# Optimization experiments

Hardware: AMD Instinct MI355X
Metric: run time of the kernel (lower is better)

The kernel has to match this reference:

```python
import jax, jax.numpy as jnp
import numpy as np

B, H, S, D = 2, 16, 2048, 64

def setup_inputs() -> dict:
    key = jax.random.key(0)
    kq, kk, kv = jax.random.split(key, 3)
    q = jax.random.normal(kq, (B, H, S, D), dtype=jnp.float32)
    k = jax.random.normal(kk, (B, H, S, D), dtype=jnp.float32)
    v = jax.random.normal(kv, (B, H, S, D), dtype=jnp.float32)
    # causal mask: True where position j > i (future tokens are masked)
    mask = jnp.triu(jnp.ones((S, S), dtype=bool), k=1)[None, None, :, :]
    return {"q": q, "k": k, "v": v, "mask": mask}

def reference(q, k, v, mask) -> jnp.ndarray:
    # scaled dot-product attention with additive -1e4 mask bias
    scale = 1.0 / jnp.sqrt(jnp.asarray(q.shape[-1], q.dtype))
    scores = jnp.einsum('bhqd,bhkd->bhqk', q, k) * scale  # [B,H,S,S]
    scores = scores + mask.astype(scores.dtype) * jnp.asarray(-10000.0, scores.dtype)
    probs = jax.nn.softmax(scores, axis=-1)
    # dropout is identity in eval mode
    return jnp.einsum('bhqk,bhkd->bhqd', probs, v)
```

## Files before the change

kernel.cpp:

```cpp
#include <hip/hip_runtime.h>

typedef __bf16 bf16_t;
typedef bf16_t bf16x8 __attribute__((ext_vector_type(8)));
typedef bf16_t bf16x4 __attribute__((ext_vector_type(4)));
typedef float  floatx4 __attribute__((ext_vector_type(4)));

constexpr int Sq = 2048, Dq = 64;
constexpr int BQ = 128, BK = 64;
constexpr int NQT = Sq / BQ;
constexpr int STR = 72;
constexpr float SCALE_LOG2E = 0.125f * 1.44269504088896340736f;

__global__ __launch_bounds__(256, 2) void flash_attn_kernel(
    const float* __restrict__ Q, const float* __restrict__ K,
    const float* __restrict__ V, float* __restrict__ O)
{
    __shared__ bf16_t QPs[BQ][STR];
    __shared__ bf16_t Ks[BK][STR];
    __shared__ bf16_t VTs[Dq][STR];

    const int tid  = threadIdx.x;
    const int wave = tid >> 6;
    const int lane = tid & 63;
    const int quad = lane >> 4;
    const int l16  = lane & 15;

    const int b  = blockIdx.x;
    const int x  = b & 255;
    const int bh = (x & 7) | (((x >> 7) & 1) << 3) | (((b >> 8) & 1) << 4);
    const int qidx = (x >> 3) & 15;
    const int qt = (b >> 8) ? (NQT - 1 - qidx) : qidx;
    const int ktmax = 2 * qt + 1;
    const long base = (long)bh * Sq * Dq;

    const int r0 = tid >> 4;
    const int c4 = (tid & 15) * 4;
    const int h  = lane >> 3;
    const int jw = wave * 16;

    #pragma unroll
    for (int p = 0; p < 8; ++p) {
        const int row = p * 16 + r0;
        const float4 qv = *(const float4*)&Q[base + (long)(qt * BQ + row) * Dq + c4];
        bf16x4 w;
        w[0] = (bf16_t)(qv.x * SCALE_LOG2E); w[1] = (bf16_t)(qv.y * SCALE_LOG2E);
        w[2] = (bf16_t)(qv.z * SCALE_LOG2E); w[3] = (bf16_t)(qv.w * SCALE_LOG2E);
        *(bf16x4*)&QPs[row][c4] = w;
    }
    __syncthreads();

    bf16x8 aq[2][2];
    #pragma unroll
    for (int u = 0; u < 2; ++u) {
        #pragma unroll
        for (int hh = 0; hh < 2; ++hh)
            aq[u][hh] = *(const bf16x8*)&QPs[32 * wave + u * 16 + l16][hh * 32 + quad * 8];
    }

    float l_lane[2] = {0.f, 0.f};
    floatx4 o_acc[2][4];
    #pragma unroll
    for (int u = 0; u < 2; ++u)
        #pragma unroll
        for (int dt = 0; dt < 4; ++dt) o_acc[u][dt] = floatx4{0.f, 0.f, 0.f, 0.f};

    float4 kf[4];
    float  vf[4][4];
    #pragma unroll
    for (int p = 0; p < 4; ++p) {
        kf[p] = *(const float4*)&K[base + (long)(p * 16 + r0) * Dq + c4];
        const int j0 = jw + 4 * ((p + h) & 3);
        #pragma unroll
        for (int r = 0; r < 4; ++r)
            vf[p][r] = V[base + (long)(j0 + r) * Dq + lane];
    }

    for (int kt = 0; kt <= ktmax; ++kt) {
        __syncthreads();

        #pragma unroll
        for (int p = 0; p < 4; ++p) {
            bf16x4 w;
            w[0] = (bf16_t)kf[p].x; w[1] = (bf16_t)kf[p].y;
            w[2] = (bf16_t)kf[p].z; w[3] = (bf16_t)kf[p].w;
            *(bf16x4*)&Ks[p * 16 + r0][c4] = w;
            bf16x4 vw;
            vw[0] = (bf16_t)vf[p][0]; vw[1] = (bf16_t)vf[p][1];
            vw[2] = (bf16_t)vf[p][2]; vw[3] = (bf16_t)vf[p][3];
            *(bf16x4*)&VTs[lane][jw + 4 * ((p + h) & 3)] = vw;
        }
        __syncthreads();

        {
            const int kn = (kt < ktmax) ? (kt + 1) : ktmax;
            const long kb = base + (long)kn * BK * Dq;
            #pragma unroll
            for (int p = 0; p < 4; ++p) {
                kf[p] = *(const float4*)&K[kb + (long)(p * 16 + r0) * Dq + c4];
                const int j0 = jw + 4 * ((p + h) & 3);
                #pragma unroll
                for (int r = 0; r < 4; ++r)
                    vf[p][r] = V[kb + (long)(j0 + r) * Dq + lane];
            }
        }

        floatx4 acc[4][2];
        #pragma unroll
        for (int t = 0; t < 4; ++t) {
            const int krow = t * 16 + l16;
            bf16x8 ak0 = *(const bf16x8*)&Ks[krow][quad * 8];
            bf16x8 ak1 = *(const bf16x8*)&Ks[krow][32 + quad * 8];
            #pragma unroll
            for (int u = 0; u < 2; ++u) {
                acc[t][u] = floatx4{0.f, 0.f, 0.f, 0.f};
                acc[t][u] = __builtin_amdgcn_mfma_f32_16x16x32_bf16(ak0, aq[u][0], acc[t][u], 0, 0, 0);
                acc[t][u] = __builtin_amdgcn_mfma_f32_16x16x32_bf16(ak1, aq[u][1], acc[t][u], 0, 0, 0);
            }
        }

        if (kt >= 2 * qt) {
            #pragma unroll
            for (int u = 0; u < 2; ++u) {
                const int qr = qt * BQ + 32 * wave + u * 16 + l16;
                #pragma unroll
                for (int t = 0; t < 4; ++t) {
                    #pragma unroll
                    for (int i = 0; i < 4; ++i) {
                        if (kt * BK + t * 16 + quad * 4 + i > qr) acc[t][u][i] = -1e30f;
                    }
                }
            }
        }

        #pragma unroll
        for (int u = 0; u < 2; ++u) {
            float l_add = 0.f;
            #pragma unroll
            for (int t = 0; t < 4; ++t) {
                #pragma unroll
                for (int i = 0; i < 4; ++i) {
                    acc[t][u][i] = __builtin_amdgcn_exp2f(acc[t][u][i]);
                    l_add += acc[t][u][i];
                }
            }
            l_lane[u] += l_add;
        }

        #pragma unroll
        for (int u = 0; u < 2; ++u) {
            #pragma unroll
            for (int t = 0; t < 4; ++t) {
                bf16x4 pk;
                pk[0] = (bf16_t)acc[t][u][0]; pk[1] = (bf16_t)acc[t][u][1];
                pk[2] = (bf16_t)acc[t][u][2]; pk[3] = (bf16_t)acc[t][u][3];
                *(bf16x4*)&QPs[32 * wave + u * 16 + l16][t * 16 + quad * 4] = pk;
            }
        }

        bf16x8 ap[2][2];
        #pragma unroll
        for (int u = 0; u < 2; ++u) {
            #pragma unroll
            for (int hh = 0; hh < 2; ++hh)
                ap[u][hh] = *(const bf16x8*)&QPs[32 * wave + u * 16 + l16][hh * 32 + quad * 8];
        }
        #pragma unroll
        for (int dt = 0; dt < 4; ++dt) {
            const int dcol = dt * 16 + l16;
            bf16x8 bv0 = *(const bf16x8*)&VTs[dcol][quad * 8];
            bf16x8 bv1 = *(const bf16x8*)&VTs[dcol][32 + quad * 8];
            #pragma unroll
            for (int u = 0; u < 2; ++u) {
                o_acc[u][dt] = __builtin_amdgcn_mfma_f32_16x16x32_bf16(ap[u][0], bv0, o_acc[u][dt], 0, 0, 0);
                o_acc[u][dt] = __builtin_amdgcn_mfma_f32_16x16x32_bf16(ap[u][1], bv1, o_acc[u][dt], 0, 0, 0);
            }
        }
    }

    #pragma unroll
    for (int u = 0; u < 2; ++u) {
        float lsum = l_lane[u];
        lsum += __shfl_xor(lsum, 16);
        lsum += __shfl_xor(lsum, 32);
        #pragma unroll
        for (int i = 0; i < 4; ++i) {
            const float inv_l = 1.f / __shfl(lsum, quad * 4 + i, 16);
            const long row = (long)qt * BQ + 32 * wave + u * 16 + quad * 4 + i;
            #pragma unroll
            for (int dt = 0; dt < 4; ++dt) {
                O[base + row * Dq + dt * 16 + l16] = o_acc[u][dt][i] * inv_l;
            }
        }
    }
}

extern "C" void kernel_launch(void* const* d_in, const int* in_sizes, int n_in,
                              void* d_out, int out_size, void* d_ws, size_t ws_size,
                              hipStream_t stream)
{
    const float* q = (const float*)d_in[0];
    const float* k = (const float*)d_in[1];
    const float* v = (const float*)d_in[2];
    float* out = (float*)d_out;
    flash_attn_kernel<<<dim3(512, 1, 1), dim3(256, 1, 1), 0, stream>>>(q, k, v, out);
}
```

Baseline: 135.1 us.

## Split causal KV range across two blocks with pairwise q-tile balancing and combine pass

```diff
diff --git a/kernel.cpp b/kernel.cpp
--- a/kernel.cpp
+++ b/kernel.cpp
@@ -11,9 +11,10 @@
 constexpr int STR = 72;
 constexpr float SCALE_LOG2E = 0.125f * 1.44269504088896340736f;
 
-__global__ __launch_bounds__(256, 2) void flash_attn_kernel(
+__global__ __launch_bounds__(256, 2) void flash_attn_splitk(
     const float* __restrict__ Q, const float* __restrict__ K,
-    const float* __restrict__ V, float* __restrict__ O)
+    const float* __restrict__ V, float* __restrict__ O,
+    float* __restrict__ wsO, float* __restrict__ wsLA, float* __restrict__ wsLB)
 {
     __shared__ bf16_t QPs[BQ][STR];
     __shared__ bf16_t Ks[BK][STR];
@@ -25,75 +26,57 @@
     const int quad = lane >> 4;
     const int l16  = lane & 15;
 
-    const int b  = blockIdx.x;
-    const int x  = b & 255;
-    const int bh = (x & 7) | (((x >> 7) & 1) << 3) | (((b >> 8) & 1) << 4);
-    const int qidx = (x >> 3) & 15;
-    const int qt = (b >> 8) ? (NQT - 1 - qidx) : qidx;
-    const int ktmax = 2 * qt + 1;
+    const int b    = blockIdx.x;
+    const int half = b >> 8;
+    const int x    = b & 255;
+    const int bh   = (x & 7) | ((x >> 6) << 3);
+    const int pair = (x >> 3) & 7;
     const long base = (long)bh * Sq * Dq;
+
+    float* __restrict__ dstO = half ? wsO  : O;
+    float* __restrict__ wsL  = half ? wsLB : wsLA;
 
     const int r0 = tid >> 4;
     const int c4 = (tid & 15) * 4;
     const int h  = lane >> 3;
     const int jw = wave * 16;
 
-    #pragma unroll
-    for (int p = 0; p < 8; ++p) {
-        const int row = p * 16 + r0;
-        const float4 qv = *(const float4*)&Q[base + (long)(qt * BQ + row) * Dq + c4];
-        bf16x4 w;
-        w[0] = (bf16_t)(qv.x * SCALE_LOG2E); w[1] = (bf16_t)(qv.y * SCALE_LOG2E);
-        w[2] = (bf16_t)(qv.z * SCALE_LOG2E); w[3] = (bf16_t)(qv.w * SCALE_LOG2E);
-        *(bf16x4*)&QPs[row][c4] = w;
-    }
-    __syncthreads();
-
-    bf16x8 aq[2][2];
-    #pragma unroll
-    for (int u = 0; u < 2; ++u) {
-        #pragma unroll
-        for (int hh = 0; hh < 2; ++hh)
-            aq[u][hh] = *(const bf16x8*)&QPs[32 * wave + u * 16 + l16][hh * 32 + quad * 8];
-    }
-
-    float l_lane[2] = {0.f, 0.f};
-    floatx4 o_acc[2][4];
-    #pragma unroll
-    for (int u = 0; u < 2; ++u)
-        #pragma unroll
-        for (int dt = 0; dt < 4; ++dt) o_acc[u][dt] = floatx4{0.f, 0.f, 0.f, 0.f};
-
-    float4 kf[4];
-    float  vf[4][4];
-    #pragma unroll
-    for (int p = 0; p < 4; ++p) {
-        kf[p] = *(const float4*)&K[base + (long)(p * 16 + r0) * Dq + c4];
-        const int j0 = jw + 4 * ((p + h) & 3);
-        #pragma unroll
-        for (int r = 0; r < 4; ++r)
-            vf[p][r] = V[base + (long)(j0 + r) * Dq + lane];
-    }
-
-    for (int kt = 0; kt <= ktmax; ++kt) {
+    for (int tt = 0; tt < 2; ++tt) {
+        const int qt   = tt ? (NQT - 1 - pair) : pair;
+        const int nkt  = qt + 1;
+        const int ktbeg = half * nkt;
+
         __syncthreads();
 
         #pragma unroll
-        for (int p = 0; p < 4; ++p) {
+        for (int p = 0; p < 8; ++p) {
+            const int row = p * 16 + r0;
+            const float4 qv = *(const float4*)&Q[base + (long)(qt * BQ + row) * Dq + c4];
             bf16x4 w;
-            w[0] = (bf16_t)kf[p].x; w[1] = (bf16_t)kf[p].y;
-            w[2] = (bf16_t)kf[p].z; w[3] = (bf16_t)kf[p].w;
-            *(bf16x4*)&Ks[p * 16 + r0][c4] = w;
-            bf16x4 vw;
-            vw[0] = (bf16_t)vf[p][0]; vw[1] = (bf16_t)vf[p][1];
-            vw[2] = (bf16_t)vf[p][2]; vw[3] = (bf16_t)vf[p][3];
-            *(bf16x4*)&VTs[lane][jw + 4 * ((p + h) & 3)] = vw;
+            w[0] = (bf16_t)(qv.x * SCALE_LOG2E); w[1] = (bf16_t)(qv.y * SCALE_LOG2E);
+            w[2] = (bf16_t)(qv.z * SCALE_LOG2E); w[3] = (bf16_t)(qv.w * SCALE_LOG2E);
+            *(bf16x4*)&QPs[row][c4] = w;
         }
         __syncthreads();
 
+        bf16x8 aq[2][2];
+        #pragma unroll
+        for (int u = 0; u < 2; ++u)
+            #pragma unroll
+            for (int hh = 0; hh < 2; ++hh)
+                aq[u][hh] = *(const bf16x8*)&QPs[32 * wave + u * 16 + l16][hh * 32 + quad * 8];
+
+        float l_lane[2] = {0.f, 0.f};
+        floatx4 o_acc[2][4];
+        #pragma unroll
+        for (int u = 0; u < 2; ++u)
+            #pragma unroll
+            for (int dt = 0; dt < 4; ++dt) o_acc[u][dt] = floatx4{0.f, 0.f, 0.f, 0.f};
+
+        float4 kf[4];
+        float  vf[4][4];
         {
-            const int kn = (kt < ktmax) ? (kt + 1) : ktmax;
-            const long kb = base + (long)kn * BK * Dq;
+            const long kb = base + (long)ktbeg * BK * Dq;
             #pragma unroll
             for (int p = 0; p < 4; ++p) {
                 kf[p] = *(const float4*)&K[kb + (long)(p * 16 + r0) * Dq + c4];
@@ -104,94 +87,141 @@
             }
         }
 
-        floatx4 acc[4][2];
-        #pragma unroll
-        for (int t = 0; t < 4; ++t) {
-            const int krow = t * 16 + l16;
-            bf16x8 ak0 = *(const bf16x8*)&Ks[krow][quad * 8];
-            bf16x8 ak1 = *(const bf16x8*)&Ks[krow][32 + quad * 8];
+        for (int j = 0; j < nkt; ++j) {
+            const int kt = ktbeg + j;
+            __syncthreads();
+
+            #pragma unroll
+            for (int p = 0; p < 4; ++p) {
+                bf16x4 w;
+                w[0] = (bf16_t)kf[p].x; w[1] = (bf16_t)kf[p].y;
+                w[2] = (bf16_t)kf[p].z; w[3] = (bf16_t)kf[p].w;
+                *(bf16x4*)&Ks[p * 16 + r0][c4] = w;
+                bf16x4 vw;
+                vw[0] = (bf16_t)vf[p][0]; vw[1] = (bf16_t)vf[p][1];
+                vw[2] = (bf16_t)vf[p][2]; vw[3] = (bf16_t)vf[p][3];
+                *(bf16x4*)&VTs[lane][jw + 4 * ((p + h) & 3)] = vw;
+            }
+            __syncthreads();
+
+            {
+                const int kn = (j + 1 < nkt) ? (kt + 1) : kt;
+                const long kb = base + (long)kn * BK * Dq;
+                #pragma unroll
+                for (int p = 0; p < 4; ++p) {
+                    kf[p] = *(const float4*)&K[kb + (long)(p * 16 + r0) * Dq + c4];
+                    const int j0 = jw + 4 * ((p + h) & 3);
+                    #pragma unroll
+                    for (int r = 0; r < 4; ++r)
+                        vf[p][r] = V[kb + (long)(j0 + r) * Dq + lane];
+                }
+            }
+
+            floatx4 acc[4][2];
+            #pragma unroll
+            for (int t = 0; t < 4; ++t) {
+                const int krow = t * 16 + l16;
+                bf16x8 ak0 = *(const bf16x8*)&Ks[krow][quad * 8];
+                bf16x8 ak1 = *(const bf16x8*)&Ks[krow][32 + quad * 8];
+                #pragma unroll
+                for (int u = 0; u < 2; ++u) {
+                    acc[t][u] = floatx4{0.f, 0.f, 0.f, 0.f};
+                    acc[t][u] = __builtin_amdgcn_mfma_f32_16x16x32_bf16(ak0, aq[u][0], acc[t][u], 0, 0, 0);
+                    acc[t][u] = __builtin_amdgcn_mfma_f32_16x16x32_bf16(ak1, aq[u][1], acc[t][u], 0, 0, 0);
+                }
+            }
+
+            if (kt >= 2 * qt) {
+                #pragma unroll
+                for (int u = 0; u < 2; ++u) {
+                    const int qr = qt * BQ + 32 * wave + u * 16 + l16;
+                    #pragma unroll
+                    for (int t = 0; t < 4; ++t) {
+                        #pragma unroll
+                        for (int i = 0; i < 4; ++i) {
+                            if (kt * BK + t * 16 + quad * 4 + i > qr) acc[t][u][i] = -1e30f;
+                        }
+                    }
+                }
+            }
+
             #pragma unroll
             for (int u = 0; u < 2; ++u) {
-                acc[t][u] = floatx4{0.f, 0.f, 0.f, 0.f};
-                acc[t][u] = __builtin_amdgcn_mfma_f32_16x16x32_bf16(ak0, aq[u][0], acc[t][u], 0, 0, 0);
-                acc[t][u] = __builtin_amdgcn_mfma_f32_16x16x32_bf16(ak1, aq[u][1], acc[t][u], 0, 0, 0);
-            }
-        }
-
-        if (kt >= 2 * qt) {
-            #pragma unroll
-            for (int u = 0; u < 2; ++u) {
-                const int qr = qt * BQ + 32 * wave + u * 16 + l16;
+                float l_add = 0.f;
                 #pragma unroll
                 for (int t = 0; t < 4; ++t) {
                     #pragma unroll
                     for (int i = 0; i < 4; ++i) {
-                        if (kt * BK + t * 16 + quad * 4 + i > qr) acc[t][u][i] = -1e30f;
+                        acc[t][u][i] = __builtin_amdgcn_exp2f(acc[t][u][i]);
+                        l_add += acc[t][u][i];
                     }
                 }
+                l_lane[u] += l_add;
+            }
+
+            #pragma unroll
+            for (int u = 0; u < 2; ++u) {
+                #pragma unroll
+                for (int t = 0; t < 4; ++t) {
+                    bf16x4 pk;
+                    pk[0] = (bf16_t)acc[t][u][0]; pk[1] = (bf16_t)acc[t][u][1];
+                    pk[2] = (bf16_t)acc[t][u][2]; pk[3] = (bf16_t)acc[t][u][3];
+                    *(bf16x4*)&QPs[32 * wave + u * 16 + l16][t * 16 + quad * 4] = pk;
+                }
+            }
+
+            bf16x8 ap[2][2];
+            #pragma unroll
+            for (int u = 0; u < 2; ++u)
+                #pragma unroll
+                for (int hh = 0; hh < 2; ++hh)
+                    ap[u][hh] = *(const bf16x8*)&QPs[32 * wave + u * 16 + l16][hh * 32 + quad * 8];
+            #pragma unroll
+            for (int dt = 0; dt < 4; ++dt) {
+                const int dcol = dt * 16 + l16;
+                bf16x8 bv0 = *(const bf16x8*)&VTs[dcol][quad * 8];
+                bf16x8 bv1 = *(const bf16x8*)&VTs[dcol][32 + quad * 8];
+                #pragma unroll
+                for (int u = 0; u < 2; ++u) {
+                    o_acc[u][dt] = __builtin_amdgcn_mfma_f32_16x16x32_bf16(ap[u][0], bv0, o_acc[u][dt], 0, 0, 0);
+                    o_acc[u][dt] = __builtin_amdgcn_mfma_f32_16x16x32_bf16(ap[u][1], bv1, o_acc[u][dt], 0, 0, 0);
+                }
             }
         }
 
         #pragma unroll
         for (int u = 0; u < 2; ++u) {
-            float l_add = 0.f;
-            #pragma unroll
-            for (int t = 0; t < 4; ++t) {
-                #pragma unroll
-                for (int i = 0; i < 4; ++i) {
-                    acc[t][u][i] = __builtin_amdgcn_exp2f(acc[t][u][i]);
-                    l_add += acc[t][u][i];
-                }
-            }
-            l_lane[u] += l_add;
-        }
-
-        #pragma unroll
-        for (int u = 0; u < 2; ++u) {
-            #pragma unroll
-            for (int t = 0; t < 4; ++t) {
-                bf16x4 pk;
-                pk[0] = (bf16_t)acc[t][u][0]; pk[1] = (bf16_t)acc[t][u][1];
-                pk[2] = (bf16_t)acc[t][u][2]; pk[3] = (bf16_t)acc[t][u][3];
-                *(bf16x4*)&QPs[32 * wave + u * 16 + l16][t * 16 + quad * 4] = pk;
-            }
-        }
-
-        bf16x8 ap[2][2];
-        #pragma unroll
-        for (int u = 0; u < 2; ++u) {
-            #pragma unroll
-            for (int hh = 0; hh < 2; ++hh)
-                ap[u][hh] = *(const bf16x8*)&QPs[32 * wave + u * 16 + l16][hh * 32 + quad * 8];
-        }
-        #pragma unroll
-        for (int dt = 0; dt < 4; ++dt) {
-            const int dcol = dt * 16 + l16;
-            bf16x8 bv0 = *(const bf16x8*)&VTs[dcol][quad * 8];
-            bf16x8 bv1 = *(const bf16x8*)&VTs[dcol][32 + quad * 8];
-            #pragma unroll
-            for (int u = 0; u < 2; ++u) {
-                o_acc[u][dt] = __builtin_amdgcn_mfma_f32_16x16x32_bf16(ap[u][0], bv0, o_acc[u][dt], 0, 0, 0);
-                o_acc[u][dt] = __builtin_amdgcn_mfma_f32_16x16x32_bf16(ap[u][1], bv1, o_acc[u][dt], 0, 0, 0);
+            float lsum = l_lane[u];
+            lsum += __shfl_xor(lsum, 16);
+            lsum += __shfl_xor(lsum, 32);
+            if (quad == 0) {
+                wsL[(bh * NQT + qt) * BQ + 32 * wave + u * 16 + l16] = lsum;
+            }
+            #pragma unroll
+            for (int i = 0; i < 4; ++i) {
+                const long row = (long)qt * BQ + 32 * wave + u * 16 + quad * 4 + i;
+                #pragma unroll
+                for (int dt = 0; dt < 4; ++dt) {
+                    dstO[base + row * Dq + dt * 16 + l16] = o_acc[u][dt][i];
+                }
             }
         }
     }
-
-    #pragma unroll
-    for (int u = 0; u < 2; ++u) {
-        float lsum = l_lane[u];
-        lsum += __shfl_xor(lsum, 16);
-        lsum += __shfl_xor(lsum, 32);
-        #pragma unroll
-        for (int i = 0; i < 4; ++i) {
-            const float inv_l = 1.f / __shfl(lsum, quad * 4 + i, 16);
-            const long row = (long)qt * BQ + 32 * wave + u * 16 + quad * 4 + i;
-            #pragma unroll
-            for (int dt = 0; dt < 4; ++dt) {
-                O[base + row * Dq + dt * 16 + l16] = o_acc[u][dt][i] * inv_l;
-            }
-        }
-    }
+}
+
+__global__ __launch_bounds__(256) void combine_kernel(
+    float* __restrict__ O, const float* __restrict__ wsO,
+    const float* __restrict__ lA, const float* __restrict__ lB)
+{
+    const int g = blockIdx.x * 256 + threadIdx.x;
+    const int row = g >> 4;
+    const float inv = 1.f / (lA[row] + lB[row]);
+    const float4 a = ((const float4*)O)[g];
+    const float4 c = ((const float4*)wsO)[g];
+    float4 r;
+    r.x = (a.x + c.x) * inv; r.y = (a.y + c.y) * inv;
+    r.z = (a.z + c.z) * inv; r.w = (a.w + c.w) * inv;
+    ((float4*)O)[g] = r;
 }
 
 extern "C" void kernel_launch(void* const* d_in, const int* in_sizes, int n_in,
@@ -202,5 +232,9 @@
     const float* k = (const float*)d_in[1];
     const float* v = (const float*)d_in[2];
     float* out = (float*)d_out;
-    flash_attn_kernel<<<dim3(512, 1, 1), dim3(256, 1, 1), 0, stream>>>(q, k, v, out);
+    float* wsO = (float*)d_ws;
+    float* lA  = wsO + 4194304;
+    float* lB  = lA + 65536;
+    flash_attn_splitk<<<dim3(512, 1, 1), dim3(256, 1, 1), 0, stream>>>(q, k, v, out, wsO, lA, lB);
+    combine_kernel<<<dim3(4096, 1, 1), dim3(256, 1, 1), 0, stream>>>(out, wsO, lA, lB);
 }
```

New measurement: 140.1 us. 3.7% more time.

## Split causal attention KV range across blocks with atomic accumulation and normalize pass

Applied to the files above, without the earlier changes.

```diff
diff --git a/kernel.cpp b/kernel.cpp
--- a/kernel.cpp
+++ b/kernel.cpp
@@ -11,9 +11,10 @@
 constexpr int STR = 72;
 constexpr float SCALE_LOG2E = 0.125f * 1.44269504088896340736f;
 
-__global__ __launch_bounds__(256, 2) void flash_attn_kernel(
+__global__ __launch_bounds__(256, 4) void flash_attn_splitk(
     const float* __restrict__ Q, const float* __restrict__ K,
-    const float* __restrict__ V, float* __restrict__ O)
+    const float* __restrict__ V, float* __restrict__ O,
+    float* __restrict__ wsL)
 {
     __shared__ bf16_t QPs[BQ][STR];
     __shared__ bf16_t Ks[BK][STR];
@@ -26,172 +27,198 @@
     const int l16  = lane & 15;
 
     const int b  = blockIdx.x;
+    const int j  = b >> 8;
     const int x  = b & 255;
-    const int bh = (x & 7) | (((x >> 7) & 1) << 3) | (((b >> 8) & 1) << 4);
-    const int qidx = (x >> 3) & 15;
-    const int qt = (b >> 8) ? (NQT - 1 - qidx) : qidx;
-    const int ktmax = 2 * qt + 1;
+    const int bh = (x & 7) | ((x >> 6) << 3);
+    const int p  = (x >> 3) & 7;
     const long base = (long)bh * Sq * Dq;
+
+    const int c0 = 9 * j - (j / 3);
+    const int c1 = c0 + 9 - (j >> 1);
+    const int sA = 2 * p + 2;
 
     const int r0 = tid >> 4;
     const int c4 = (tid & 15) * 4;
     const int h  = lane >> 3;
     const int jw = wave * 16;
 
-    #pragma unroll
-    for (int p = 0; p < 8; ++p) {
-        const int row = p * 16 + r0;
-        const float4 qv = *(const float4*)&Q[base + (long)(qt * BQ + row) * Dq + c4];
-        bf16x4 w;
-        w[0] = (bf16_t)(qv.x * SCALE_LOG2E); w[1] = (bf16_t)(qv.y * SCALE_LOG2E);
-        w[2] = (bf16_t)(qv.z * SCALE_LOG2E); w[3] = (bf16_t)(qv.w * SCALE_LOG2E);
-        *(bf16x4*)&QPs[row][c4] = w;
-    }
-    __syncthreads();
-
-    bf16x8 aq[2][2];
-    #pragma unroll
-    for (int u = 0; u < 2; ++u) {
-        #pragma unroll
-        for (int hh = 0; hh < 2; ++hh)
-            aq[u][hh] = *(const bf16x8*)&QPs[32 * wave + u * 16 + l16][hh * 32 + quad * 8];
-    }
-
-    float l_lane[2] = {0.f, 0.f};
-    floatx4 o_acc[2][4];
-    #pragma unroll
-    for (int u = 0; u < 2; ++u)
-        #pragma unroll
-        for (int dt = 0; dt < 4; ++dt) o_acc[u][dt] = floatx4{0.f, 0.f, 0.f, 0.f};
-
-    float4 kf[4];
-    float  vf[4][4];
-    #pragma unroll
-    for (int p = 0; p < 4; ++p) {
-        kf[p] = *(const float4*)&K[base + (long)(p * 16 + r0) * Dq + c4];
-        const int j0 = jw + 4 * ((p + h) & 3);
-        #pragma unroll
-        for (int r = 0; r < 4; ++r)
-            vf[p][r] = V[base + (long)(j0 + r) * Dq + lane];
-    }
-
-    for (int kt = 0; kt <= ktmax; ++kt) {
+    for (int seg = 0; seg < 2; ++seg) {
+        int qt, k0, k1;
+        if (seg == 0) { qt = p;           k0 = c0;                    k1 = (c1 < sA) ? c1 : sA; }
+        else          { qt = NQT - 1 - p; k0 = (c0 > sA ? c0 : sA) - sA; k1 = c1 - sA; }
+        if (k0 >= k1) continue;
+
         __syncthreads();
 
         #pragma unroll
-        for (int p = 0; p < 4; ++p) {
+        for (int pp = 0; pp < 8; ++pp) {
+            const int row = pp * 16 + r0;
+            const float4 qv = *(const float4*)&Q[base + (long)(qt * BQ + row) * Dq + c4];
             bf16x4 w;
-            w[0] = (bf16_t)kf[p].x; w[1] = (bf16_t)kf[p].y;
-            w[2] = (bf16_t)kf[p].z; w[3] = (bf16_t)kf[p].w;
-            *(bf16x4*)&Ks[p * 16 + r0][c4] = w;
-            bf16x4 vw;
-            vw[0] = (bf16_t)vf[p][0]; vw[1] = (bf16_t)vf[p][1];
-            vw[2] = (bf16_t)vf[p][2]; vw[3] = (bf16_t)vf[p][3];
-            *(bf16x4*)&VTs[lane][jw + 4 * ((p + h) & 3)] = vw;
+            w[0] = (bf16_t)(qv.x * SCALE_LOG2E); w[1] = (bf16_t)(qv.y * SCALE_LOG2E);
+            w[2] = (bf16_t)(qv.z * SCALE_LOG2E); w[3] = (bf16_t)(qv.w * SCALE_LOG2E);
+            *(bf16x4*)&QPs[row][c4] = w;
         }
         __syncthreads();
 
+        bf16x8 aq[2][2];
+        #pragma unroll
+        for (int u = 0; u < 2; ++u)
+            #pragma unroll
+            for (int hh = 0; hh < 2; ++hh)
+                aq[u][hh] = *(const bf16x8*)&QPs[32 * wave + u * 16 + l16][hh * 32 + quad * 8];
+
+        float l_lane[2] = {0.f, 0.f};
+        floatx4 o_acc[2][4];
+        #pragma unroll
+        for (int u = 0; u < 2; ++u)
+            #pragma unroll
+            for (int dt = 0; dt < 4; ++dt) o_acc[u][dt] = floatx4{0.f, 0.f, 0.f, 0.f};
+
+        float4 kf[4];
+        float  vf[4][4];
         {
-            const int kn = (kt < ktmax) ? (kt + 1) : ktmax;
-            const long kb = base + (long)kn * BK * Dq;
-            #pragma unroll
-            for (int p = 0; p < 4; ++p) {
-                kf[p] = *(const float4*)&K[kb + (long)(p * 16 + r0) * Dq + c4];
-                const int j0 = jw + 4 * ((p + h) & 3);
+            const long kb = base + (long)k0 * BK * Dq;
+            #pragma unroll
+            for (int pp = 0; pp < 4; ++pp) {
+                kf[pp] = *(const float4*)&K[kb + (long)(pp * 16 + r0) * Dq + c4];
+                const int j0 = jw + 4 * ((pp + h) & 3);
                 #pragma unroll
                 for (int r = 0; r < 4; ++r)
-                    vf[p][r] = V[kb + (long)(j0 + r) * Dq + lane];
-            }
-        }
-
-        floatx4 acc[4][2];
-        #pragma unroll
-        for (int t = 0; t < 4; ++t) {
-            const int krow = t * 16 + l16;
-            bf16x8 ak0 = *(const bf16x8*)&Ks[krow][quad * 8];
-            bf16x8 ak1 = *(const bf16x8*)&Ks[krow][32 + quad * 8];
+                    vf[pp][r] = V[kb + (long)(j0 + r) * Dq + lane];
+            }
+        }
+
+        for (int kt = k0; kt < k1; ++kt) {
+            __syncthreads();
+
+            #pragma unroll
+            for (int pp = 0; pp < 4; ++pp) {
+                bf16x4 w;
+                w[0] = (bf16_t)kf[pp].x; w[1] = (bf16_t)kf[pp].y;
+                w[2] = (bf16_t)kf[pp].z; w[3] = (bf16_t)kf[pp].w;
+                *(bf16x4*)&Ks[pp * 16 + r0][c4] = w;
+                bf16x4 vw;
+                vw[0] = (bf16_t)vf[pp][0]; vw[1] = (bf16_t)vf[pp][1];
+                vw[2] = (bf16_t)vf[pp][2]; vw[3] = (bf16_t)vf[pp][3];
+                *(bf16x4*)&VTs[lane][jw + 4 * ((pp + h) & 3)] = vw;
+            }
+            __syncthreads();
+
+            {
+                const int kn = (kt + 1 < k1) ? (kt + 1) : kt;
+                const long kb = base + (long)kn * BK * Dq;
+                #pragma unroll
+                for (int pp = 0; pp < 4; ++pp) {
+                    kf[pp] = *(const float4*)&K[kb + (long)(pp * 16 + r0) * Dq + c4];
+                    const int j0 = jw + 4 * ((pp + h) & 3);
+                    #pragma unroll
+                    for (int r = 0; r < 4; ++r)
+                        vf[pp][r] = V[kb + (long)(j0 + r) * Dq + lane];
+                }
+            }
+
+            floatx4 acc[4][2];
+            #pragma unroll
+            for (int t = 0; t < 4; ++t) {
+                const int krow = t * 16 + l16;
+                bf16x8 ak0 = *(const bf16x8*)&Ks[krow][quad * 8];
+                bf16x8 ak1 = *(const bf16x8*)&Ks[krow][32 + quad * 8];
+                #pragma unroll
+                for (int u = 0; u < 2; ++u) {
+                    acc[t][u] = floatx4{0.f, 0.f, 0.f, 0.f};
+                    acc[t][u] = __builtin_amdgcn_mfma_f32_16x16x32_bf16(ak0, aq[u][0], acc[t][u], 0, 0, 0);
+                    acc[t][u] = __builtin_amdgcn_mfma_f32_16x16x32_bf16(ak1, aq[u][1], acc[t][u], 0, 0, 0);
+                }
+            }
+
+            if (kt >= 2 * qt) {
+                #pragma unroll
+                for (int u = 0; u < 2; ++u) {
+                    const int qr = qt * BQ + 32 * wave + u * 16 + l16;
+                    #pragma unroll
+                    for (int t = 0; t < 4; ++t) {
+                        #pragma unroll
+                        for (int i = 0; i < 4; ++i) {
+                            if (kt * BK + t * 16 + quad * 4 + i > qr) acc[t][u][i] = -1e30f;
+                        }
+                    }
+                }
+            }
+
             #pragma unroll
             for (int u = 0; u < 2; ++u) {
-                acc[t][u] = floatx4{0.f, 0.f, 0.f, 0.f};
-                acc[t][u] = __builtin_amdgcn_mfma_f32_16x16x32_bf16(ak0, aq[u][0], acc[t][u], 0, 0, 0);
-                acc[t][u] = __builtin_amdgcn_mfma_f32_16x16x32_bf16(ak1, aq[u][1], acc[t][u], 0, 0, 0);
-            }
-        }
-
-        if (kt >= 2 * qt) {
-            #pragma unroll
-            for (int u = 0; u < 2; ++u) {
-                const int qr = qt * BQ + 32 * wave + u * 16 + l16;
+                float l_add = 0.f;
                 #pragma unroll
                 for (int t = 0; t < 4; ++t) {
                     #pragma unroll
                     for (int i = 0; i < 4; ++i) {
-                        if (kt * BK + t * 16 + quad * 4 + i > qr) acc[t][u][i] = -1e30f;
+                        acc[t][u][i] = __builtin_amdgcn_exp2f(acc[t][u][i]);
+                        l_add += acc[t][u][i];
                     }
                 }
+                l_lane[u] += l_add;
+            }
+
+            #pragma unroll
+            for (int u = 0; u < 2; ++u) {
+                #pragma unroll
+                for (int t = 0; t < 4; ++t) {
+                    bf16x4 pk;
+                    pk[0] = (bf16_t)acc[t][u][0]; pk[1] = (bf16_t)acc[t][u][1];
+                    pk[2] = (bf16_t)acc[t][u][2]; pk[3] = (bf16_t)acc[t][u][3];
+                    *(bf16x4*)&QPs[32 * wave + u * 16 + l16][t * 16 + quad * 4] = pk;
+                }
+            }
+
+            bf16x8 ap[2][2];
+            #pragma unroll
+            for (int u = 0; u < 2; ++u)
+                #pragma unroll
+                for (int hh = 0; hh < 2; ++hh)
+                    ap[u][hh] = *(const bf16x8*)&QPs[32 * wave + u * 16 + l16][hh * 32 + quad * 8];
+            #pragma unroll
+            for (int dt = 0; dt < 4; ++dt) {
+                const int dcol = dt * 16 + l16;
+                bf16x8 bv0 = *(const bf16x8*)&VTs[dcol][quad * 8];
+                bf16x8 bv1 = *(const bf16x8*)&VTs[dcol][32 + quad * 8];
+                #pragma unroll
+                for (int u = 0; u < 2; ++u) {
+                    o_acc[u][dt] = __builtin_amdgcn_mfma_f32_16x16x32_bf16(ap[u][0], bv0, o_acc[u][dt], 0, 0, 0);
+                    o_acc[u][dt] = __builtin_amdgcn_mfma_f32_16x16x32_bf16(ap[u][1], bv1, o_acc[u][dt], 0, 0, 0);
+                }
             }
         }
 
         #pragma unroll
         for (int u = 0; u < 2; ++u) {
-            float l_add = 0.f;
-            #pragma unroll
-            for (int t = 0; t < 4; ++t) {
-                #pragma unroll
-                for (int i = 0; i < 4; ++i) {
-                    acc[t][u][i] = __builtin_amdgcn_exp2f(acc[t][u][i]);
-                    l_add += acc[t][u][i];
-                }
-            }
-            l_lane[u] += l_add;
-        }
-
-        #pragma unroll
-        for (int u = 0; u < 2; ++u) {
-            #pragma unroll
-            for (int t = 0; t < 4; ++t) {
-                bf16x4 pk;
-                pk[0] = (bf16_t)acc[t][u][0]; pk[1] = (bf16_t)acc[t][u][1];
-                pk[2] = (bf16_t)acc[t][u][2]; pk[3] = (bf16_t)acc[t][u][3];
-                *(bf16x4*)&QPs[32 * wave + u * 16 + l16][t * 16 + quad * 4] = pk;
-            }
-        }
-
-        bf16x8 ap[2][2];
-        #pragma unroll
-        for (int u = 0; u < 2; ++u) {
-            #pragma unroll
-            for (int hh = 0; hh < 2; ++hh)
-                ap[u][hh] = *(const bf16x8*)&QPs[32 * wave + u * 16 + l16][hh * 32 + quad * 8];
-        }
-        #pragma unroll
-        for (int dt = 0; dt < 4; ++dt) {
-            const int dcol = dt * 16 + l16;
-            bf16x8 bv0 = *(const bf16x8*)&VTs[dcol][quad * 8];
-            bf16x8 bv1 = *(const bf16x8*)&VTs[dcol][32 + quad * 8];
-            #pragma unroll
-            for (int u = 0; u < 2; ++u) {
-                o_acc[u][dt] = __builtin_amdgcn_mfma_f32_16x16x32_bf16(ap[u][0], bv0, o_acc[u][dt], 0, 0, 0);
-                o_acc[u][dt] = __builtin_amdgcn_mfma_f32_16x16x32_bf16(ap[u][1], bv1, o_acc[u][dt], 0, 0, 0);
+            float lsum = l_lane[u];
+            lsum += __shfl_xor(lsum, 16);
+            lsum += __shfl_xor(lsum, 32);
+            if (quad == 0) {
+                atomicAdd(&wsL[(bh * NQT + qt) * BQ + 32 * wave + u * 16 + l16], lsum);
+            }
+            #pragma unroll
+            for (int i = 0; i < 4; ++i) {
+                const long row = (long)qt * BQ + 32 * wave + u * 16 + quad * 4 + i;
+                #pragma unroll
+                for (int dt = 0; dt < 4; ++dt) {
+                    atomicAdd(&O[base + row * Dq + dt * 16 + l16], o_acc[u][dt][i]);
+                }
             }
         }
     }
-
-    #pragma unroll
-    for (int u = 0; u < 2; ++u) {
-        float lsum = l_lane[u];
-        lsum += __shfl_xor(lsum, 16);
-        lsum += __shfl_xor(lsum, 32);
-        #pragma unroll
-        for (int i = 0; i < 4; ++i) {
-            const float inv_l = 1.f / __shfl(lsum, quad * 4 + i, 16);
-            const long row = (long)qt * BQ + 32 * wave + u * 16 + quad * 4 + i;
-            #pragma unroll
-            for (int dt = 0; dt < 4; ++dt) {
-                O[base + row * Dq + dt * 16 + l16] = o_acc[u][dt][i] * inv_l;
-            }
-        }
-    }
+}
+
+__global__ __launch_bounds__(256) void normalize_kernel(
+    float* __restrict__ O, const float* __restrict__ wsL)
+{
+    const int g = blockIdx.x * 256 + threadIdx.x;
+    const int row = g >> 4;
+    const float inv = 1.f / wsL[row];
+    float4 v = ((const float4*)O)[g];
+    v.x *= inv; v.y *= inv; v.z *= inv; v.w *= inv;
+    ((float4*)O)[g] = v;
 }
 
 extern "C" void kernel_launch(void* const* d_in, const int* in_sizes, int n_in,
@@ -202,5 +229,9 @@
     const float* k = (const float*)d_in[1];
     const float* v = (const float*)d_in[2];
     float* out = (float*)d_out;
-    flash_attn_kernel<<<dim3(512, 1, 1), dim3(256, 1, 1), 0, stream>>>(q, k, v, out);
+    float* wsL = (float*)d_ws;
+    hipMemsetAsync(out, 0, (size_t)out_size * sizeof(float), stream);
+    hipMemsetAsync(wsL, 0, 65536 * sizeof(float), stream);
+    flash_attn_splitk<<<dim3(1024, 1, 1), dim3(256, 1, 1), 0, stream>>>(q, k, v, out, wsL);
+    normalize_kernel<<<dim3(4096, 1, 1), dim3(256, 1, 1), 0, stream>>>(out, wsL);
 }
```

Measured after the change: 228.1 us. 1.69x slower.
